# Kernel optimization log

Hardware: AMD Instinct MI355X
Metric: run time of the kernel (lower is better)

## Reference

```python
import jax, jax.numpy as jnp
import numpy as np

B, S, D = 2, 2048, 1024
H = 16
HD = D // H


def setup_inputs() -> dict:
    key = jax.random.key(0)
    k1, k2, k3 = jax.random.split(key, 3)
    x = jax.random.normal(k1, (B, S, D), dtype=jnp.float32)
    # xavier_uniform for qkv (fan_in=D, fan_out=3D) and out (D,D)
    lim_qkv = float(np.sqrt(6.0 / (D + 3 * D)))
    lim_out = float(np.sqrt(6.0 / (D + D)))
    W_qkv = jax.random.uniform(k2, (D, 3 * D), dtype=jnp.float32, minval=-lim_qkv, maxval=lim_qkv)
    b_qkv = jnp.zeros((3 * D,), dtype=jnp.float32)
    W_out = jax.random.uniform(k3, (D, D), dtype=jnp.float32, minval=-lim_out, maxval=lim_out)
    b_out = jnp.zeros((D,), dtype=jnp.float32)
    return {"x": x, "W_qkv": W_qkv, "b_qkv": b_qkv, "W_out": W_out, "b_out": b_out}


def reference(x, W_qkv, b_qkv, W_out, b_out):
    bs, seq_len, _ = x.shape
    qkv = x @ W_qkv + b_qkv                                  # [B,S,3D]
    qkv = qkv.reshape(bs, seq_len, H, 3 * HD).transpose(0, 2, 1, 3)  # [B,H,S,3HD]
    q, k, v = jnp.split(qkv, 3, axis=-1)                     # each [B,H,S,HD]
    score = jnp.einsum('bhqd,bhkd->bhqk', q, k) / jnp.sqrt(jnp.float32(HD))
    # Faithful to the torch code: mask float has -inf on strict upper triangle,
    # masked_fill treats nonzero (-inf) as True and fills with -9e-13 (~0),
    # so non-causal positions get logit -9e-13, NOT -inf.
    upper = jnp.triu(jnp.ones((seq_len, seq_len), dtype=bool), k=1)  # [S,S]
    score = jnp.where(upper, jnp.float32(-9e-13), score)
    score = jax.nn.softmax(score, axis=-1)
    value = jnp.einsum('bhqk,bhkd->bhqd', score, v)          # [B,H,S,HD]
    value = value.transpose(0, 2, 1, 3).reshape(bs, seq_len, D)
    out = value @ W_out + b_out                              # dropout p=0 (eval)
    return out
```

## Files before the change

### kernel.cpp

```cpp
#include <hip/hip_runtime.h>
#include <math.h>

#define B_ 2
#define S_ 2048
#define D_ 1024
#define H_ 16
#define HD_ 64

typedef unsigned short ushort8 __attribute__((ext_vector_type(8)));
typedef unsigned int u32x4 __attribute__((ext_vector_type(4)));
typedef _Float16 f16x8 __attribute__((ext_vector_type(8)));
typedef _Float16 f16x2 __attribute__((ext_vector_type(2)));
typedef float f32x4 __attribute__((ext_vector_type(4)));

__device__ __forceinline__ unsigned short f2h(float f) {
    union { _Float16 h; unsigned short u; } v;
    v.h = (_Float16)f;
    return v.u;
}
__device__ __forceinline__ float h2f(unsigned short u) {
    union { unsigned short u; _Float16 h; } v; v.u = u;
    return (float)v.h;
}
__device__ __forceinline__ ushort8 pack2x4h(f32x4 a, f32x4 b) {
    ushort8 hi;
    #pragma unroll
    for (int i = 0; i < 4; ++i) { hi[i] = f2h(a[i]); hi[4 + i] = f2h(b[i]); }
    return hi;
}

#define SWZ(row, col) ((((row)) << 6) + (((col)) ^ ((((row)) & 7) << 3)))

__device__ __forceinline__ f32x4 mfma16(f16x8 a, f16x8 b, f32x4 c) {
    return __builtin_amdgcn_mfma_f32_16x16x32_f16(a, b, c, 0, 0, 0);
}

typedef __attribute__((address_space(1))) const void gvoid_t;
typedef __attribute__((address_space(3))) void lvoid_t;
typedef __attribute__((address_space(3))) unsigned short lds_us_t;
__device__ __forceinline__ void gload_lds16(const void* g, void* l) {
    __builtin_amdgcn_global_load_lds((gvoid_t*)g, (lvoid_t*)l, 16, 0, 0);
}
__device__ __forceinline__ f16x8 dsr128(unsigned addr) {
    u32x4 r;
    asm volatile("ds_read_b128 %0, %1" : "=v"(r) : "v"(addr));
    union { u32x4 u; f16x8 h; } cv; cv.u = r; return cv.h;
}

__global__ __launch_bounds__(256) void conv_rows_kernel(
    const float* __restrict__ in, unsigned short* __restrict__ ohi)
{
    const int id = blockIdx.x * 256 + threadIdx.x;
    const int r = id >> 7, c = id & 127;
    const float* s = in + (size_t)r * 1024 + c * 8;
    f32x4 v0 = *(const f32x4*)s, v1 = *(const f32x4*)(s + 4);
    ushort8 hi = pack2x4h(v0, v1);
    const int oc = (c & ~7) | ((c ^ r) & 7);
    *(ushort8*)&ohi[(size_t)r * 1024 + oc * 8] = hi;
}

__global__ __launch_bounds__(256) void conv_wt_kernel(
    const float* __restrict__ Wq, const float* __restrict__ Wo,
    unsigned short* __restrict__ Wqh, unsigned short* __restrict__ Woh)
{
    __shared__ float T[64][65];
    const float* W; int ldw, ny;
    unsigned short *oh;
    if (blockIdx.y < 48) { W = Wq; ldw = 3072; ny = blockIdx.y * 64; oh = Wqh; }
    else                 { W = Wo; ldw = 1024; ny = (blockIdx.y - 48) * 64; oh = Woh; }
    const int tid = threadIdx.x;
    const int kx = blockIdx.x * 64;
    const int kl = tid >> 2, c0 = (tid & 3) * 16;
    const float* s = W + (size_t)(kx + kl) * ldw + ny + c0;
    #pragma unroll
    for (int i = 0; i < 4; ++i) *(f32x4*)&T[kl][c0 + 4 * i] = *(const f32x4*)(s + 4 * i);
    __syncthreads();
    const int nl = tid >> 2, jj = (tid & 3) * 2;
    #pragma unroll
    for (int p = 0; p < 2; ++p) {
        const int j = jj + p;
        f32x4 a, b;
        #pragma unroll
        for (int i = 0; i < 4; ++i) a[i] = T[j * 8 + i][nl];
        #pragma unroll
        for (int i = 0; i < 4; ++i) b[i] = T[j * 8 + 4 + i][nl];
        ushort8 hi = pack2x4h(a, b);
        const int row = ny + nl;
        const int chunk = blockIdx.x * 8 + (j ^ (nl & 7));
        *(ushort8*)&oh[(size_t)row * 1024 + chunk * 8] = hi;
    }
}

template<int OUTMODE>
__global__ __launch_bounds__(256, 4) void gemm16_kernel(
    const unsigned short* __restrict__ Ah, const unsigned short* __restrict__ Bth,
    const float* __restrict__ bias, float* __restrict__ Cf, float* __restrict__ Cf1,
    unsigned short* __restrict__ Ohi,
    int M, int N, int K)
{
    __shared__ __align__(16) unsigned short lds[16384];

    const int tid = threadIdx.x, lane = tid & 63, w = tid >> 6;
    const int wm = w >> 1, wn = w & 1;
    const int gx = gridDim.x, nwg = gx * gridDim.y;
    const int lin = blockIdx.y * gx + blockIdx.x;
    const int nl = (lin & 7) * (nwg >> 3) + (lin >> 3);
    int mblk = nl / gx;
    int koff = 0;
    float* Cfw = Cf;
    bool dobias = (OUTMODE != 2);
    if (OUTMODE == 2) {
        const int halfrows = (int)(gridDim.y >> 1);
        if (mblk >= halfrows) { mblk -= halfrows; koff = 512; Cfw = Cf1; dobias = false; }
        else dobias = true;
    }
    const int m0 = mblk * 128, n0 = (nl % gx) * 128;
    const int col = lane & 15, g = lane >> 4;
    const int NT = K >> 5;

    const int sr0 = (w * 2 + 0) * 16 + (lane >> 2);
    const int sr1 = (w * 2 + 1) * 16 + (lane >> 2);
    const int scp = lane & 3;

    auto stage = [&](int tt) {
        unsigned short* dst = &lds[(tt & 1) * 8192];
        const int hi8 = (tt >> 1) * 8;
        const int tb4 = (tt & 1) << 2;
        #pragma unroll
        for (int q = 0; q < 2; ++q) {
            const int r = q ? sr1 : sr0;
            const int p = hi8 + ((tb4 ^ (r & 4)) | (scp ^ ((r >> 2) & 3)));
            const size_t go = (size_t)p * 8 + koff;
            const int slotb = (w * 2 + q) * 512;
            gload_lds16(Ah  + (size_t)(m0 + r) * 1024 + go, dst + 0    + slotb);
            gload_lds16(Bth + (size_t)(n0 + r) * 1024 + go, dst + 4096 + slotb);
        }
    };

    const unsigned ldsb = (unsigned)(size_t)(lds_us_t*)lds;
    const unsigned sk = (unsigned)(((g ^ (col & 3) ^ ((col >> 2) & 3)) & 3) << 4);
    const unsigned aB = ldsb + (unsigned)((wm * 64 + col) * 64) + sk;
    const unsigned bB = ldsb + 8192u + (unsigned)((wn * 64 + col) * 64) + sk;

    f32x4 acc[4][4] = {};

    stage(0);
    stage(1);

    for (int tt = 0; tt < NT; ++tt) {
        if (tt + 1 < NT) asm volatile("s_waitcnt vmcnt(4)" ::: "memory");
        else             asm volatile("s_waitcnt vmcnt(0)" ::: "memory");
        __builtin_amdgcn_s_barrier();
        __builtin_amdgcn_sched_barrier(0);
        const unsigned bo = (unsigned)((tt & 1) * 16384);

        f16x8 a[4], b[4];
        #pragma unroll
        for (int i = 0; i < 4; ++i) a[i] = dsr128(aB + bo + i * 1024u);
        #pragma unroll
        for (int i = 0; i < 4; ++i) b[i] = dsr128(bB + bo + i * 1024u);

        asm volatile("s_waitcnt lgkmcnt(0)" ::: "memory");
        __builtin_amdgcn_sched_barrier(0);
        __builtin_amdgcn_s_setprio(1);
        #pragma unroll
        for (int mi = 0; mi < 4; ++mi)
            #pragma unroll
            for (int nj = 0; nj < 4; ++nj)
                acc[mi][nj] = mfma16(a[mi], b[nj], acc[mi][nj]);
        __builtin_amdgcn_s_setprio(0);
        __builtin_amdgcn_s_barrier();
        __builtin_amdgcn_sched_barrier(0);
        if (tt + 2 < NT) stage(tt + 2);
    }

    __syncthreads();
    float* ow = (float*)((char*)lds + w * 8192);
    const int nc = (lane & 7) * 8;
    const int nabs = n0 + wn * 64 + nc;
    f32x4 bi0 = {}, bi1 = {};
    if (dobias) { bi0 = *(const f32x4*)&bias[nabs]; bi1 = *(const f32x4*)&bias[nabs + 4]; }
    #pragma unroll
    for (int half = 0; half < 2; ++half) {
        __builtin_amdgcn_wave_barrier();
        #pragma unroll
        for (int ml = 0; ml < 2; ++ml)
            #pragma unroll
            for (int nj = 0; nj < 4; ++nj)
                #pragma unroll
                for (int r = 0; r < 4; ++r)
                    ow[(ml * 16 + g * 4 + r) * 64 + nj * 16 + col] = acc[half * 2 + ml][nj][r];
        __builtin_amdgcn_wave_barrier();
        #pragma unroll
        for (int it = 0; it < 4; ++it) {
            const int rl = it * 8 + (lane >> 3);
            f32x4 v0 = *(const f32x4*)&ow[rl * 64 + nc];
            f32x4 v1 = *(const f32x4*)&ow[rl * 64 + nc + 4];
            if (dobias) { v0 += bi0; v1 += bi1; }
            const int m = m0 + wm * 64 + half * 32 + rl;
            if (OUTMODE == 1) {
                ushort8 hi = pack2x4h(v0, v1);
                const int chunk = (lane & 7) ^ (m & 7);
                *(ushort8*)&Ohi[(size_t)m * N + n0 + wn * 64 + chunk * 8] = hi;
            } else {
                *(f32x4*)&Cfw[(size_t)m * N + nabs] = v0;
                *(f32x4*)&Cfw[(size_t)m * N + nabs + 4] = v1;
            }
        }
        __builtin_amdgcn_wave_barrier();
    }
}

__global__ __launch_bounds__(256) void addp_kernel(
    float* __restrict__ out, const float* __restrict__ p1)
{
    const size_t idx = ((size_t)blockIdx.x * 256 + threadIdx.x) * 4;
    f32x4 v = *(const f32x4*)&out[idx];
    f32x4 u = *(const f32x4*)&p1[idx];
    v += u;
    *(f32x4*)&out[idx] = v;
}

__global__ __launch_bounds__(256) void vsuf_part_kernel(
    const unsigned short* __restrict__ qh, float* __restrict__ tsum)
{
    const int bh = blockIdx.x, tg = blockIdx.y;
    const int b = bh >> 4, h = bh & 15;
    const unsigned short* qhB = qh + (size_t)b * 2048 * 3072;
    const int tl = threadIdx.x >> 6, lane = threadIdx.x & 63;
    const int t = tg * 4 + tl;
    const int dgrp = lane & 7, rr = lane >> 3;
    const int colbase = h * 192 + 128;
    float sacc[8] = {};
    for (int kk = 0; kk < 8; ++kk) {
        const int row = t * 64 + rr + kk * 8;
        const size_t off = (size_t)row * 3072 + colbase + ((dgrp ^ rr) << 3);
        ushort8 vh = *(const ushort8*)&qhB[off];
        #pragma unroll
        for (int e = 0; e < 8; ++e) sacc[e] += h2f(vh[e]);
    }
    #pragma unroll
    for (int off = 8; off < 64; off <<= 1)
        #pragma unroll
        for (int e = 0; e < 8; ++e) sacc[e] += __shfl_xor(sacc[e], off);
    if (rr == 0) {
        float* dst = &tsum[((size_t)bh * 32 + t) * 64 + dgrp * 8];
        f32x4 v0, v1;
        #pragma unroll
        for (int e = 0; e < 4; ++e) { v0[e] = sacc[e]; v1[e] = sacc[4 + e]; }
        *(f32x4*)dst = v0;
        *(f32x4*)(dst + 4) = v1;
    }
}

__global__ __launch_bounds__(64) void vsuf_scan_kernel(
    const float* __restrict__ tsum, float* __restrict__ vsuf)
{
    const int bh = blockIdx.x, d = threadIdx.x;
    float acc = 0.f;
    vsuf[((size_t)bh * 33 + 32) * 64 + d] = 0.f;
    for (int t = 31; t >= 0; --t) {
        acc += tsum[((size_t)bh * 32 + t) * 64 + d];
        vsuf[((size_t)bh * 33 + t) * 64 + d] = acc;
    }
}

__global__ __launch_bounds__(256, 4) void attn_kernel(
    const unsigned short* __restrict__ qh,
    const float* __restrict__ vsuf,
    unsigned short* __restrict__ ohi,
    float* __restrict__ partO, float* __restrict__ partML)
{
    __shared__ __align__(16) unsigned short lds[16384];

    const int tid = threadIdx.x, lane = tid & 63, w = tid >> 6;
    const int g = lane >> 4, oct = g * 8, col = lane & 15;
    const int bh = blockIdx.y;
    const int b = bh >> 4, h = bh & 15;
    const unsigned short* qhB = qh + (size_t)b * 2048 * 3072;
    const float* vsufB = vsuf + (size_t)bh * 33 * 64;
    const int brow = b * 2048;
    const int kp = tid & 31, dg = tid >> 5;

    const int job = blockIdx.x;
    int i, s = 0, slot = -1;
    if (job < 32) { const int r = job; i = 16 + (r >> 1); s = r & 1; slot = (bh << 5) + r; }
    else { i = 47 - job; }
    const int q0 = i * 64;
    const int ntile_all = i + 1;
    const int t_begin = s * 16;
    const int t_end = (slot < 0) ? ntile_all : min(t_begin + 16, ntile_all);
    const bool isseg = (slot >= 0);

    auto kissue = [&](int ktbase, ushort8* kr) {
        #pragma unroll
        for (int j = 0; j < 2; ++j) {
            const int cc = w * 2 + j;
            const int row = ktbase + cc * 8 + (lane >> 3);
            kr[j] = *(const ushort8*)(qhB + (size_t)row * 3072 + h * 192 + 64 + (lane & 7) * 8);
        }
    };
    auto kwrite = [&](const ushort8* kr) {
        #pragma unroll
        for (int j = 0; j < 2; ++j) {
            const int cc = w * 2 + j;
            *(ushort8*)&lds[cc * 512 + lane * 8] = kr[j];
        }
    };
    auto vload = [&](int ktbase, f16x8& vA, f16x8& vB) {
        const int r0 = ktbase + 2 * kp, r1 = r0 + 1;
        const int pA = dg ^ (r0 & 7), pB = dg ^ (r1 & 7);
        vA = *(const f16x8*)&qhB[(size_t)r0 * 3072 + h * 192 + 128 + pA * 8];
        vB = *(const f16x8*)&qhB[(size_t)r1 * 3072 + h * 192 + 128 + pB * 8];
    };
    auto vwrite = [&](f16x8 vA, f16x8 vB) {
        #pragma unroll
        for (int e = 0; e < 8; ++e) {
            const int d = dg * 8 + e;
            f16x2 pr; pr[0] = vA[e]; pr[1] = vB[e];
            *(f16x2*)&lds[8192 + SWZ(d, 2 * kp)] = pr;
        }
    };

    #pragma unroll
    for (int j = 0; j < 2; ++j) {
        const int cc = w * 2 + j;
        const int row = q0 + cc * 8 + (lane >> 3);
        gload_lds16(qhB + (size_t)row * 3072 + h * 192 + (lane & 7) * 8,
                    &lds[cc * 512]);
    }
    ushort8 kr[2]; f16x8 vA, vB;
    kissue(t_begin * 64, kr);
    vload(t_begin * 64, vA, vB);
    __syncthreads();
    f16x8 qfh[2];
    {
        const int qrow = w * 16 + col;
        qfh[0] = *(const f16x8*)&lds[SWZ(qrow, oct)];
        qfh[1] = *(const f16x8*)&lds[SWZ(qrow, 32 + oct)];
    }
    __syncthreads();
    kwrite(kr);
    vwrite(vA, vB);
    __syncthreads();

    const int qg = q0 + w * 16 + col;
    float l_run = 0.f;
    f32x4 oacc[4] = {};

    for (int t = t_begin; t < t_end; ++t) {
        const int kt = t * 64;
        const bool pf = (t + 1 < t_end);
        if (pf) { kissue(kt + 64, kr); vload(kt + 64, vA, vB); }

        f32x4 sacc[4] = {};
        #pragma unroll
        for (int c = 0; c < 2; ++c)
            #pragma unroll
            for (int t4 = 0; t4 < 4; ++t4) {
                const int krow = t4 * 16 + col;
                f16x8 khf = *(const f16x8*)&lds[SWZ(krow, c * 32 + oct)];
                sacc[t4] = mfma16(khf, qfh[c], sacc[t4]);
            }

        unsigned short* Pw = &lds[12288 + w * 1024];
        if (t == ntile_all - 1) {
            #pragma unroll
            for (int t4 = 0; t4 < 4; ++t4)
                #pragma unroll
                for (int rp = 0; rp < 2; ++rp) {
                    const int k0 = kt + t4 * 16 + g * 4 + rp * 2;
                    float s0 = sacc[t4][rp * 2]     * 0.125f;
                    float s1 = sacc[t4][rp * 2 + 1] * 0.125f;
                    if (k0 > qg)     s0 = 0.0f;
                    if (k0 + 1 > qg) s1 = 0.0f;
                    float e0 = __expf(s0), e1 = __expf(s1);
                    l_run += e0 + e1;
                    f16x2 pk; pk[0] = (_Float16)e0; pk[1] = (_Float16)e1;
                    *(f16x2*)&Pw[SWZ(col, t4 * 16 + g * 4 + rp * 2)] = pk;
                }
        } else {
            #pragma unroll
            for (int t4 = 0; t4 < 4; ++t4)
                #pragma unroll
                for (int rp = 0; rp < 2; ++rp) {
                    float e0 = __expf(sacc[t4][rp * 2]     * 0.125f);
                    float e1 = __expf(sacc[t4][rp * 2 + 1] * 0.125f);
                    l_run += e0 + e1;
                    f16x2 pk; pk[0] = (_Float16)e0; pk[1] = (_Float16)e1;
                    *(f16x2*)&Pw[SWZ(col, t4 * 16 + g * 4 + rp * 2)] = pk;
                }
        }

        __builtin_amdgcn_wave_barrier();

        __syncthreads();
        if (pf) kwrite(kr);

        #pragma unroll
        for (int c = 0; c < 2; ++c) {
            f16x8 pfv = *(const f16x8*)&Pw[SWZ(col, c * 32 + oct)];
            #pragma unroll
            for (int dt = 0; dt < 4; ++dt) {
                f16x8 vh = *(const f16x8*)&lds[8192 + SWZ(dt * 16 + col, c * 32 + oct)];
                oacc[dt] = mfma16(vh, pfv, oacc[dt]);
            }
        }

        __syncthreads();
        if (pf) vwrite(vA, vB);
    }

    float lt = l_run;
    lt += __shfl_xor(lt, 16);
    lt += __shfl_xor(lt, 32);

    if (isseg) {
        float* po = partO + (size_t)slot * 4096;
        #pragma unroll
        for (int dt = 0; dt < 4; ++dt)
            #pragma unroll
            for (int r = 0; r < 4; ++r)
                po[(dt * 16 + g * 4 + r) * 64 + w * 16 + col] = oacc[dt][r];
        if (g == 0) partML[(size_t)slot * 128 + w * 16 + col] = lt;
        return;
    }

    lt += (float)(S_ - q0 - 64);
    {
        const float* vs = vsufB + (size_t)(i + 1) * 64;
        #pragma unroll
        for (int dt = 0; dt < 4; ++dt)
            #pragma unroll
            for (int r = 0; r < 4; ++r)
                oacc[dt][r] += vs[dt * 16 + g * 4 + r];
    }
    const float inv = 1.f / lt;
    float* ow = (float*)&lds[w * 4096];
    const int q = lane >> 2, jj = lane & 3;
    #pragma unroll
    for (int half = 0; half < 2; ++half) {
        __builtin_amdgcn_wave_barrier();
        #pragma unroll
        for (int t4 = 0; t4 < 2; ++t4)
            #pragma unroll
            for (int r = 0; r < 4; ++r)
                ow[col * 40 + t4 * 16 + g * 4 + r] = oacc[half * 2 + t4][r] * inv;
        __builtin_amdgcn_wave_barrier();
        f32x4 v0 = *(const f32x4*)&ow[q * 40 + jj * 8];
        f32x4 v1 = *(const f32x4*)&ow[q * 40 + jj * 8 + 4];
        ushort8 hi = pack2x4h(v0, v1);
        const int m = brow + q0 + w * 16 + q;
        const int chunk = (half * 4 + jj) ^ (m & 7);
        *(ushort8*)&ohi[(size_t)m * 1024 + h * 64 + chunk * 8] = hi;
    }
}

__global__ __launch_bounds__(256) void attn_combine_kernel(
    const float* __restrict__ partO, const float* __restrict__ partML,
    const float* __restrict__ vsuf,
    unsigned short* __restrict__ ohi)
{
    const int i = 16 + blockIdx.x;
    const int bh = blockIdx.y;
    const int b = bh >> 4, h = bh & 15;
    const float* vsufB = vsuf + (size_t)bh * 33 * 64;
    const int brow = b * 2048;
    const int nseg = 2;
    const int slot0 = (bh << 5) + (i - 16) * 2;
    const int q = threadIdx.x & 63, dgrp = threadIdx.x >> 6;
    const int q0 = i * 64;

    float lstar = (float)(S_ - q0 - 64);

    float od[16];
    const float* vs = vsufB + (size_t)(i + 1) * 64 + dgrp * 16;
    #pragma unroll
    for (int k = 0; k < 16; ++k) od[k] = vs[k];

    for (int sg = 0; sg < nseg; ++sg) {
        lstar += partML[(size_t)(slot0 + sg) * 128 + q];
        const float* po = partO + (size_t)(slot0 + sg) * 4096 + (size_t)(dgrp * 16) * 64 + q;
        #pragma unroll
        for (int k = 0; k < 16; ++k) od[k] += po[k * 64];
    }

    const float inv = 1.f / lstar;
    f32x4 a0, a1, b0, b1;
    #pragma unroll
    for (int k = 0; k < 4; ++k) {
        a0[k] = od[k] * inv; a1[k] = od[4 + k] * inv;
        b0[k] = od[8 + k] * inv; b1[k] = od[12 + k] * inv;
    }
    ushort8 hi0 = pack2x4h(a0, a1);
    ushort8 hi1 = pack2x4h(b0, b1);
    const int mrow = brow + q0 + q;
    const int c0 = (dgrp * 2) ^ (mrow & 7);
    const int c1 = (dgrp * 2 + 1) ^ (mrow & 7);
    const size_t base = (size_t)mrow * 1024 + h * 64;
    *(ushort8*)&ohi[base + c0 * 8] = hi0;
    *(ushort8*)&ohi[base + c1 * 8] = hi1;
}

extern "C" void kernel_launch(void* const* d_in, const int* in_sizes, int n_in,
                              void* d_out, int out_size, void* d_ws, size_t ws_size,
                              hipStream_t stream) {
    const float* x     = (const float*)d_in[0];
    const float* W_qkv = (const float*)d_in[1];
    const float* b_qkv = (const float*)d_in[2];
    const float* W_out = (const float*)d_in[3];
    const float* b_out = (const float*)d_in[4];
    float* out = (float*)d_out;

    unsigned short* us  = (unsigned short*)d_ws;
    unsigned short* Wqh = us;
    unsigned short* Woh = Wqh + (size_t)3072 * 1024;
    unsigned short* XAhi = Woh + (size_t)1024 * 1024;
    unsigned short* QKVh = XAhi + (size_t)4096 * 1024;
    float* tsum   = (float*)(QKVh + (size_t)4096 * 3072);
    float* vsuf   = tsum + (size_t)32 * 32 * 64;
    float* partML = vsuf + (size_t)32 * 33 * 64;

    float* partO = out;
    float* p1    = (float*)QKVh;

    conv_wt_kernel<<<dim3(16, 64), 256, 0, stream>>>(W_qkv, W_out, Wqh, Woh);
    conv_rows_kernel<<<dim3(2048), 256, 0, stream>>>(x, XAhi);

    gemm16_kernel<1><<<dim3(24, 32), 256, 0, stream>>>(
        XAhi, Wqh, b_qkv, nullptr, nullptr, QKVh, 4096, 3072, 1024);

    vsuf_part_kernel<<<dim3(32, 8), 256, 0, stream>>>(QKVh, tsum);
    vsuf_scan_kernel<<<dim3(32), 64, 0, stream>>>(tsum, vsuf);

    attn_kernel<<<dim3(48, 32), 256, 0, stream>>>(
        QKVh, vsuf, XAhi, partO, partML);
    attn_combine_kernel<<<dim3(16, 32), 256, 0, stream>>>(
        partO, partML, vsuf, XAhi);

    gemm16_kernel<2><<<dim3(8, 64), 256, 0, stream>>>(
        XAhi, Woh, b_out, out, p1, nullptr, 4096, 1024, 512);
    addp_kernel<<<dim3(4096), 256, 0, stream>>>(out, p1);
}
```

Measured before the change: 133.6 us.

## Process 128-row query tiles per attention block to reuse K/V across two subtiles

New measurement: 172.0 us. 28.7% more time.

```diff
diff --git a/kernel.cpp b/kernel.cpp
--- a/kernel.cpp
+++ b/kernel.cpp
@@ -46,6 +46,8 @@
     asm volatile("ds_read_b128 %0, %1" : "=v"(r) : "v"(addr));
     union { u32x4 u; f16x8 h; } cv; cv.u = r; return cv.h;
 }
+
+#define EXPSC 0.18033688011f
 
 __global__ __launch_bounds__(256) void conv_rows_kernel(
     const float* __restrict__ in, unsigned short* __restrict__ ohi)
@@ -283,28 +285,28 @@
     const int kp = tid & 31, dg = tid >> 5;
 
     const int job = blockIdx.x;
-    int i, s = 0, slot = -1;
-    if (job < 32) { const int r = job; i = 16 + (r >> 1); s = r & 1; slot = (bh << 5) + r; }
-    else { i = 47 - job; }
-    const int q0 = i * 64;
-    const int ntile_all = i + 1;
+    int j, s = 0, slot = -1;
+    if (job < 16) { const int r = job; j = 8 + (r >> 1); s = r & 1; slot = (bh << 4) + r; }
+    else { j = 23 - job; }
+    const int q0 = j * 128;
+    const int ntile_all = 2 * j + 2;
     const int t_begin = s * 16;
     const int t_end = (slot < 0) ? ntile_all : min(t_begin + 16, ntile_all);
     const bool isseg = (slot >= 0);
 
     auto kissue = [&](int ktbase, ushort8* kr) {
         #pragma unroll
-        for (int j = 0; j < 2; ++j) {
-            const int cc = w * 2 + j;
+        for (int jj = 0; jj < 2; ++jj) {
+            const int cc = w * 2 + jj;
             const int row = ktbase + cc * 8 + (lane >> 3);
-            kr[j] = *(const ushort8*)(qhB + (size_t)row * 3072 + h * 192 + 64 + (lane & 7) * 8);
+            kr[jj] = *(const ushort8*)(qhB + (size_t)row * 3072 + h * 192 + 64 + (lane & 7) * 8);
         }
     };
     auto kwrite = [&](const ushort8* kr) {
         #pragma unroll
-        for (int j = 0; j < 2; ++j) {
-            const int cc = w * 2 + j;
-            *(ushort8*)&lds[cc * 512 + lane * 8] = kr[j];
+        for (int jj = 0; jj < 2; ++jj) {
+            const int cc = w * 2 + jj;
+            *(ushort8*)&lds[cc * 512 + lane * 8] = kr[jj];
         }
     };
     auto vload = [&](int ktbase, f16x8& vA, f16x8& vB) {
@@ -323,8 +325,8 @@
     };
 
     #pragma unroll
-    for (int j = 0; j < 2; ++j) {
-        const int cc = w * 2 + j;
+    for (int j4 = 0; j4 < 4; ++j4) {
+        const int cc = w * 4 + j4;
         const int row = q0 + cc * 8 + (lane >> 3);
         gload_lds16(qhB + (size_t)row * 3072 + h * 192 + (lane & 7) * 8,
                     &lds[cc * 512]);
@@ -333,77 +335,87 @@
     kissue(t_begin * 64, kr);
     vload(t_begin * 64, vA, vB);
     __syncthreads();
-    f16x8 qfh[2];
-    {
-        const int qrow = w * 16 + col;
-        qfh[0] = *(const f16x8*)&lds[SWZ(qrow, oct)];
-        qfh[1] = *(const f16x8*)&lds[SWZ(qrow, 32 + oct)];
+    f16x8 qf[2][2];
+    #pragma unroll
+    for (int qa = 0; qa < 2; ++qa) {
+        const int qrow = qa * 64 + w * 16 + col;
+        qf[qa][0] = *(const f16x8*)&lds[SWZ(qrow, oct)];
+        qf[qa][1] = *(const f16x8*)&lds[SWZ(qrow, 32 + oct)];
     }
     __syncthreads();
     kwrite(kr);
     vwrite(vA, vB);
     __syncthreads();
 
-    const int qg = q0 + w * 16 + col;
-    float l_run = 0.f;
-    f32x4 oacc[4] = {};
+    const int qgbase = q0 + w * 16 + col;
+    float lsum[2] = {0.f, 0.f};
+    f32x4 oacc[2][4] = {};
 
     for (int t = t_begin; t < t_end; ++t) {
         const int kt = t * 64;
         const bool pf = (t + 1 < t_end);
         if (pf) { kissue(kt + 64, kr); vload(kt + 64, vA, vB); }
 
-        f32x4 sacc[4] = {};
-        #pragma unroll
-        for (int c = 0; c < 2; ++c)
-            #pragma unroll
-            for (int t4 = 0; t4 < 4; ++t4) {
-                const int krow = t4 * 16 + col;
-                f16x8 khf = *(const f16x8*)&lds[SWZ(krow, c * 32 + oct)];
-                sacc[t4] = mfma16(khf, qfh[c], sacc[t4]);
+        const bool diag = (t >= ntile_all - 2);
+
+        #pragma unroll
+        for (int qa = 0; qa < 2; ++qa) {
+            f32x4 sacc[4] = {};
+            #pragma unroll
+            for (int c = 0; c < 2; ++c)
+                #pragma unroll
+                for (int t4 = 0; t4 < 4; ++t4) {
+                    const int krow = t4 * 16 + col;
+                    f16x8 khf = *(const f16x8*)&lds[SWZ(krow, c * 32 + oct)];
+                    sacc[t4] = mfma16(khf, qf[qa][c], sacc[t4]);
+                }
+            unsigned short* Pw = &lds[(qa ? 12288 : 4096) + w * 1024];
+            float lr = 0.f;
+            if (diag) {
+                const int qg = qgbase + qa * 64;
+                #pragma unroll
+                for (int t4 = 0; t4 < 4; ++t4)
+                    #pragma unroll
+                    for (int rp = 0; rp < 2; ++rp) {
+                        const int k0 = kt + t4 * 16 + g * 4 + rp * 2;
+                        float s0 = sacc[t4][rp * 2]     * EXPSC;
+                        float s1 = sacc[t4][rp * 2 + 1] * EXPSC;
+                        if (k0 > qg)     s0 = 0.0f;
+                        if (k0 + 1 > qg) s1 = 0.0f;
+                        float e0 = exp2f(s0), e1 = exp2f(s1);
+                        lr += e0 + e1;
+                        f16x2 pk; pk[0] = (_Float16)e0; pk[1] = (_Float16)e1;
+                        *(f16x2*)&Pw[SWZ(col, t4 * 16 + g * 4 + rp * 2)] = pk;
+                    }
+            } else {
+                #pragma unroll
+                for (int t4 = 0; t4 < 4; ++t4)
+                    #pragma unroll
+                    for (int rp = 0; rp < 2; ++rp) {
+                        float e0 = exp2f(sacc[t4][rp * 2]     * EXPSC);
+                        float e1 = exp2f(sacc[t4][rp * 2 + 1] * EXPSC);
+                        lr += e0 + e1;
+                        f16x2 pk; pk[0] = (_Float16)e0; pk[1] = (_Float16)e1;
+                        *(f16x2*)&Pw[SWZ(col, t4 * 16 + g * 4 + rp * 2)] = pk;
+                    }
             }
-
-        unsigned short* Pw = &lds[12288 + w * 1024];
-        if (t == ntile_all - 1) {
-            #pragma unroll
-            for (int t4 = 0; t4 < 4; ++t4)
-                #pragma unroll
-                for (int rp = 0; rp < 2; ++rp) {
-                    const int k0 = kt + t4 * 16 + g * 4 + rp * 2;
-                    float s0 = sacc[t4][rp * 2]     * 0.125f;
-                    float s1 = sacc[t4][rp * 2 + 1] * 0.125f;
-                    if (k0 > qg)     s0 = 0.0f;
-                    if (k0 + 1 > qg) s1 = 0.0f;
-                    float e0 = __expf(s0), e1 = __expf(s1);
-                    l_run += e0 + e1;
-                    f16x2 pk; pk[0] = (_Float16)e0; pk[1] = (_Float16)e1;
-                    *(f16x2*)&Pw[SWZ(col, t4 * 16 + g * 4 + rp * 2)] = pk;
-                }
-        } else {
-            #pragma unroll
-            for (int t4 = 0; t4 < 4; ++t4)
-                #pragma unroll
-                for (int rp = 0; rp < 2; ++rp) {
-                    float e0 = __expf(sacc[t4][rp * 2]     * 0.125f);
-                    float e1 = __expf(sacc[t4][rp * 2 + 1] * 0.125f);
-                    l_run += e0 + e1;
-                    f16x2 pk; pk[0] = (_Float16)e0; pk[1] = (_Float16)e1;
-                    *(f16x2*)&Pw[SWZ(col, t4 * 16 + g * 4 + rp * 2)] = pk;
-                }
-        }
-
-        __builtin_amdgcn_wave_barrier();
+            lsum[qa] += lr;
+        }
 
         __syncthreads();
         if (pf) kwrite(kr);
 
         #pragma unroll
-        for (int c = 0; c < 2; ++c) {
-            f16x8 pfv = *(const f16x8*)&Pw[SWZ(col, c * 32 + oct)];
-            #pragma unroll
-            for (int dt = 0; dt < 4; ++dt) {
-                f16x8 vh = *(const f16x8*)&lds[8192 + SWZ(dt * 16 + col, c * 32 + oct)];
-                oacc[dt] = mfma16(vh, pfv, oacc[dt]);
+        for (int qa = 0; qa < 2; ++qa) {
+            unsigned short* Pw = &lds[(qa ? 12288 : 4096) + w * 1024];
+            #pragma unroll
+            for (int c = 0; c < 2; ++c) {
+                f16x8 pfv = *(const f16x8*)&Pw[SWZ(col, c * 32 + oct)];
+                #pragma unroll
+                for (int dt = 0; dt < 4; ++dt) {
+                    f16x8 vh = *(const f16x8*)&lds[8192 + SWZ(dt * 16 + col, c * 32 + oct)];
+                    oacc[qa][dt] = mfma16(vh, pfv, oacc[qa][dt]);
+                }
             }
         }
 
@@ -411,48 +423,56 @@
         if (pf) vwrite(vA, vB);
     }
 
-    float lt = l_run;
-    lt += __shfl_xor(lt, 16);
-    lt += __shfl_xor(lt, 32);
+    #pragma unroll
+    for (int qa = 0; qa < 2; ++qa) {
+        lsum[qa] += __shfl_xor(lsum[qa], 16);
+        lsum[qa] += __shfl_xor(lsum[qa], 32);
+    }
 
     if (isseg) {
-        float* po = partO + (size_t)slot * 4096;
+        float* po = partO + (size_t)slot * 8192;
+        #pragma unroll
+        for (int qa = 0; qa < 2; ++qa)
+            #pragma unroll
+            for (int dt = 0; dt < 4; ++dt)
+                #pragma unroll
+                for (int r = 0; r < 4; ++r)
+                    po[(dt * 16 + g * 4 + r) * 128 + qa * 64 + w * 16 + col] = oacc[qa][dt][r];
+        if (g == 0) {
+            partML[(size_t)slot * 128 + w * 16 + col] = lsum[0];
+            partML[(size_t)slot * 128 + 64 + w * 16 + col] = lsum[1];
+        }
+        return;
+    }
+
+    const float tailc = (float)(S_ - q0 - 128);
+    const float* vs = vsufB + (size_t)ntile_all * 64;
+    const int q = lane >> 2, jj = lane & 3;
+    #pragma unroll
+    for (int qa = 0; qa < 2; ++qa) {
         #pragma unroll
         for (int dt = 0; dt < 4; ++dt)
             #pragma unroll
             for (int r = 0; r < 4; ++r)
-                po[(dt * 16 + g * 4 + r) * 64 + w * 16 + col] = oacc[dt][r];
-        if (g == 0) partML[(size_t)slot * 128 + w * 16 + col] = lt;
-        return;
-    }
-
-    lt += (float)(S_ - q0 - 64);
-    {
-        const float* vs = vsufB + (size_t)(i + 1) * 64;
-        #pragma unroll
-        for (int dt = 0; dt < 4; ++dt)
-            #pragma unroll
-            for (int r = 0; r < 4; ++r)
-                oacc[dt][r] += vs[dt * 16 + g * 4 + r];
-    }
-    const float inv = 1.f / lt;
-    float* ow = (float*)&lds[w * 4096];
-    const int q = lane >> 2, jj = lane & 3;
-    #pragma unroll
-    for (int half = 0; half < 2; ++half) {
-        __builtin_amdgcn_wave_barrier();
-        #pragma unroll
-        for (int t4 = 0; t4 < 2; ++t4)
-            #pragma unroll
-            for (int r = 0; r < 4; ++r)
-                ow[col * 40 + t4 * 16 + g * 4 + r] = oacc[half * 2 + t4][r] * inv;
-        __builtin_amdgcn_wave_barrier();
-        f32x4 v0 = *(const f32x4*)&ow[q * 40 + jj * 8];
-        f32x4 v1 = *(const f32x4*)&ow[q * 40 + jj * 8 + 4];
-        ushort8 hi = pack2x4h(v0, v1);
-        const int m = brow + q0 + w * 16 + q;
-        const int chunk = (half * 4 + jj) ^ (m & 7);
-        *(ushort8*)&ohi[(size_t)m * 1024 + h * 64 + chunk * 8] = hi;
+                oacc[qa][dt][r] += vs[dt * 16 + g * 4 + r];
+        const float inv = 1.f / (lsum[qa] + tailc);
+        float* ow = (float*)&lds[w * 4096];
+        #pragma unroll
+        for (int half = 0; half < 2; ++half) {
+            __builtin_amdgcn_wave_barrier();
+            #pragma unroll
+            for (int t4 = 0; t4 < 2; ++t4)
+                #pragma unroll
+                for (int r = 0; r < 4; ++r)
+                    ow[col * 40 + t4 * 16 + g * 4 + r] = oacc[qa][half * 2 + t4][r] * inv;
+            __builtin_amdgcn_wave_barrier();
+            f32x4 v0 = *(const f32x4*)&ow[q * 40 + jj * 8];
+            f32x4 v1 = *(const f32x4*)&ow[q * 40 + jj * 8 + 4];
+            ushort8 hi = pack2x4h(v0, v1);
+            const int m = brow + q0 + qa * 64 + w * 16 + q;
+            const int chunk = (half * 4 + jj) ^ (m & 7);
+            *(ushort8*)&ohi[(size_t)m * 1024 + h * 64 + chunk * 8] = hi;
+        }
     }
 }
 
@@ -461,45 +481,44 @@
     const float* __restrict__ vsuf,
     unsigned short* __restrict__ ohi)
 {
-    const int i = 16 + blockIdx.x;
+    const int j = 8 + blockIdx.x;
     const int bh = blockIdx.y;
     const int b = bh >> 4, h = bh & 15;
     const float* vsufB = vsuf + (size_t)bh * 33 * 64;
     const int brow = b * 2048;
-    const int nseg = 2;
-    const int slot0 = (bh << 5) + (i - 16) * 2;
-    const int q = threadIdx.x & 63, dgrp = threadIdx.x >> 6;
-    const int q0 = i * 64;
-
-    float lstar = (float)(S_ - q0 - 64);
-
-    float od[16];
-    const float* vs = vsufB + (size_t)(i + 1) * 64 + dgrp * 16;
-    #pragma unroll
-    for (int k = 0; k < 16; ++k) od[k] = vs[k];
-
-    for (int sg = 0; sg < nseg; ++sg) {
-        lstar += partML[(size_t)(slot0 + sg) * 128 + q];
-        const float* po = partO + (size_t)(slot0 + sg) * 4096 + (size_t)(dgrp * 16) * 64 + q;
-        #pragma unroll
-        for (int k = 0; k < 16; ++k) od[k] += po[k * 64];
+    const int slot0 = (bh << 4) + (j - 8) * 2;
+    const int q = threadIdx.x & 127, dgrp = threadIdx.x >> 7;
+    const int q0 = j * 128;
+    const int ntile = 2 * j + 2;
+
+    float lstar = (float)(S_ - q0 - 128)
+                + partML[(size_t)slot0 * 128 + q]
+                + partML[(size_t)(slot0 + 1) * 128 + q];
+
+    float od[32];
+    const float* vs = vsufB + (size_t)ntile * 64 + dgrp * 32;
+    #pragma unroll
+    for (int k = 0; k < 32; ++k) od[k] = vs[k];
+    #pragma unroll
+    for (int sg = 0; sg < 2; ++sg) {
+        const float* po = partO + (size_t)(slot0 + sg) * 8192 + (size_t)(dgrp * 32) * 128 + q;
+        #pragma unroll
+        for (int k = 0; k < 32; ++k) od[k] += po[k * 128];
     }
 
     const float inv = 1.f / lstar;
-    f32x4 a0, a1, b0, b1;
-    #pragma unroll
-    for (int k = 0; k < 4; ++k) {
-        a0[k] = od[k] * inv; a1[k] = od[4 + k] * inv;
-        b0[k] = od[8 + k] * inv; b1[k] = od[12 + k] * inv;
-    }
-    ushort8 hi0 = pack2x4h(a0, a1);
-    ushort8 hi1 = pack2x4h(b0, b1);
     const int mrow = brow + q0 + q;
-    const int c0 = (dgrp * 2) ^ (mrow & 7);
-    const int c1 = (dgrp * 2 + 1) ^ (mrow & 7);
     const size_t base = (size_t)mrow * 1024 + h * 64;
-    *(ushort8*)&ohi[base + c0 * 8] = hi0;
-    *(ushort8*)&ohi[base + c1 * 8] = hi1;
+    #pragma unroll
+    for (int cc = 0; cc < 4; ++cc) {
+        f32x4 a, bv;
+        #pragma unroll
+        for (int k = 0; k < 4; ++k) { a[k] = od[cc * 8 + k] * inv; bv[k] = od[cc * 8 + 4 + k] * inv; }
+        ushort8 hi = pack2x4h(a, bv);
+        const int c = dgrp * 4 + cc;
+        const int phys = c ^ (mrow & 7);
+        *(ushort8*)&ohi[base + phys * 8] = hi;
+    }
 }
 
 extern "C" void kernel_launch(void* const* d_in, const int* in_sizes, int n_in,
@@ -533,9 +552,9 @@
     vsuf_part_kernel<<<dim3(32, 8), 256, 0, stream>>>(QKVh, tsum);
     vsuf_scan_kernel<<<dim3(32), 64, 0, stream>>>(tsum, vsuf);
 
-    attn_kernel<<<dim3(48, 32), 256, 0, stream>>>(
+    attn_kernel<<<dim3(24, 32), 256, 0, stream>>>(
         QKVh, vsuf, XAhi, partO, partML);
-    attn_combine_kernel<<<dim3(16, 32), 256, 0, stream>>>(
+    attn_combine_kernel<<<dim3(8, 32), 256, 0, stream>>>(
         partO, partML, vsuf, XAhi);
 
     gemm16_kernel<2><<<dim3(8, 64), 256, 0, stream>>>(
```
